# Optimization experiments

Measured on AMD Instinct MI355X. Metric: run time of the kernel, lower is better.

## Reference

```python
import jax, jax.numpy as jnp
import numpy as np

NUM_HEADS = 16
NUM_KV_HEADS = 8
HEAD_DIM = 256
HIDDEN = 2048
ROT_DIM = 64          # head_dim * partial_rotary_factor (0.25)
RMS_EPS = 1e-6
ROPE_THETA = 10000.0
SEQ = 2048


def _rmsnorm(x, weight=None):
    # Gemma RMSNorm: x * rsqrt(mean(x^2)+eps) * (1 + w); v_norm has no scale.
    var = jnp.mean(jnp.square(x), axis=-1, keepdims=True)
    n = x * jax.lax.rsqrt(var + RMS_EPS)
    if weight is not None:
        n = n * (1.0 + weight)
    return n


def _rope(x, positions):
    # Partial neox-style RoPE on the first ROT_DIM dims of each head.
    # x: [S, H, D]
    rot, rest = x[..., :ROT_DIM], x[..., ROT_DIM:]
    half = ROT_DIM // 2
    inv_freq = 1.0 / (ROPE_THETA ** (jnp.arange(0, ROT_DIM, 2, dtype=jnp.float32) / ROT_DIM))
    freqs = positions.astype(jnp.float32)[:, None] * inv_freq  # [S, half]
    cos = jnp.cos(freqs)[:, None, :]  # [S, 1, half]
    sin = jnp.sin(freqs)[:, None, :]
    x1, x2 = rot[..., :half], rot[..., half:]
    rot_out = jnp.concatenate([x1 * cos - x2 * sin, x2 * cos + x1 * sin], axis=-1)
    return jnp.concatenate([rot_out, rest], axis=-1)


def setup_inputs() -> dict:
    key = jax.random.key(0)
    k1, k2, k3, k4, k5 = jax.random.split(key, 5)
    q_size = NUM_HEADS * HEAD_DIM
    kv_size = NUM_KV_HEADS * HEAD_DIM
    return {
        "positions": jnp.arange(SEQ, dtype=jnp.int32),
        "hidden_states": jax.random.normal(k1, (SEQ, HIDDEN), dtype=jnp.float32),
        "w_qkv": jax.random.normal(k2, (q_size + 2 * kv_size, HIDDEN), dtype=jnp.float32) * (HIDDEN ** -0.5),
        "q_norm_w": jax.random.normal(k3, (HEAD_DIM,), dtype=jnp.float32) * 0.02,
        "k_norm_w": jax.random.normal(k4, (HEAD_DIM,), dtype=jnp.float32) * 0.02,
        "w_o": jax.random.normal(k5, (HIDDEN, q_size), dtype=jnp.float32) * (q_size ** -0.5),
    }


def reference(positions, hidden_states, w_qkv, q_norm_w, k_norm_w, w_o):
    S = hidden_states.shape[0]
    q_size = NUM_HEADS * HEAD_DIM
    kv_size = NUM_KV_HEADS * HEAD_DIM

    qkv = hidden_states @ w_qkv.T  # [S, q+2kv]
    q, k, v = jnp.split(qkv, [q_size, q_size + kv_size], axis=-1)
    q = q.reshape(S, NUM_HEADS, HEAD_DIM)
    k = k.reshape(S, NUM_KV_HEADS, HEAD_DIM)
    v = v.reshape(S, NUM_KV_HEADS, HEAD_DIM)

    # per-head RMSNorms (v_norm: scale_shift=0, with_scale=False -> pure norm)
    q = _rmsnorm(q, q_norm_w)
    k = _rmsnorm(k, k_norm_w)
    v = _rmsnorm(v, None)

    q = _rope(q, positions)
    k = _rope(k, positions)

    # GQA: repeat kv heads to match query heads
    rep = NUM_HEADS // NUM_KV_HEADS
    k = jnp.repeat(k, rep, axis=1)  # [S, H, D]
    v = jnp.repeat(v, rep, axis=1)

    # RadixAttention constructed with scaling=1.0 -> no 1/sqrt(d) scale
    scores = jnp.einsum("qhd,khd->hqk", q, k)  # [H, S, S]
    causal = positions[:, None] >= positions[None, :]  # [S, S]
    scores = jnp.where(causal[None, :, :], scores, jnp.float32(-1e30))
    attn = jax.nn.softmax(scores, axis=-1)
    out = jnp.einsum("hqk,khd->qhd", attn, v)  # [S, H, D]
    out = out.reshape(S, q_size)
    return out @ w_o.T  # [S, HIDDEN]
```

## Files before the change

kernel.cpp:

```cpp
#include <hip/hip_runtime.h>
#include <stdint.h>
#include <math.h>

#define SEQ 2048
#define HID 2048
#define NH 16
#define NKV 8
#define HD 256
#define QSZ 4096
#define QKVN 8192

typedef __attribute__((ext_vector_type(4))) float f32x4;
typedef _Float16 f16x8 __attribute__((ext_vector_type(8)));
typedef unsigned short u16;

__device__ __forceinline__ u16 f2h(float f) {
  _Float16 h = (_Float16)f;
  return __builtin_bit_cast(u16, h);
}
__device__ __forceinline__ float h2f(u16 b) {
  return (float)__builtin_bit_cast(_Float16, b);
}
__device__ __forceinline__ void glds16(const void* g, void* l) {
  __builtin_amdgcn_global_load_lds(
      (const __attribute__((address_space(1))) uint32_t*)g,
      (__attribute__((address_space(3))) uint32_t*)l, 16, 0, 0);
}

__global__ void cvt_f32_f16(const float* __restrict__ in, u16* __restrict__ out, int n4) {
  int i = blockIdx.x * 256 + threadIdx.x;
  if (i < n4) {
    float4 v = reinterpret_cast<const float4*>(in)[i];
    ushort4 o = make_ushort4(f2h(v.x), f2h(v.y), f2h(v.z), f2h(v.w));
    reinterpret_cast<ushort4*>(out)[i] = o;
  }
}

template <int F16OUT>
__global__ __launch_bounds__(256, 2) void gemm_bt(
    const u16* __restrict__ A, const u16* __restrict__ B, void* __restrict__ Cv,
    int M, int N, int K) {
  __shared__ __align__(16) u16 As[128 * 32];
  __shared__ __align__(16) u16 Bs[128 * 32];
  const int t = threadIdx.x;
  const int w = t >> 6, l = t & 63;
  const int bm = blockIdx.y * 128, bn = blockIdx.x * 128;
  const int wr = (w >> 1) * 64, wc = (w & 1) * 64;
  f32x4 acc[4][4] = {};

  const int arow = t >> 2;
  const int acol = (t & 3) * 8;
  const u16* Ag0 = A + (size_t)(bm + arow) * K + acol;
  const u16* Ag1 = A + (size_t)(bm + 64 + arow) * K + acol;
  const u16* Bg0 = B + (size_t)(bn + arow) * K + acol;
  const u16* Bg1 = B + (size_t)(bn + 64 + arow) * K + acol;
  u16* Al0 = As + w * 512;
  u16* Al1 = As + 2048 + w * 512;
  u16* Bl0 = Bs + w * 512;
  u16* Bl1 = Bs + 2048 + w * 512;

  const int lr = l & 15;
  const int lko = (l >> 4) * 8;

  for (int k0 = 0; k0 < K; k0 += 32) {
    __syncthreads();
    glds16(Ag0 + k0, Al0);
    glds16(Ag1 + k0, Al1);
    glds16(Bg0 + k0, Bl0);
    glds16(Bg1 + k0, Bl1);
    __syncthreads();
    f16x8 a[4], b[4];
#pragma unroll
    for (int m = 0; m < 4; ++m) a[m] = *(const f16x8*)&As[(wr + m * 16 + lr) * 32 + lko];
#pragma unroll
    for (int n = 0; n < 4; ++n) b[n] = *(const f16x8*)&Bs[(wc + n * 16 + lr) * 32 + lko];
#pragma unroll
    for (int m = 0; m < 4; ++m)
#pragma unroll
      for (int n = 0; n < 4; ++n)
        acc[m][n] = __builtin_amdgcn_mfma_f32_16x16x32_f16(a[m], b[n], acc[m][n], 0, 0, 0);
  }

#pragma unroll
  for (int m = 0; m < 4; ++m) {
#pragma unroll
    for (int n = 0; n < 4; ++n) {
      const int col = bn + wc + n * 16 + lr;
      const int row0 = bm + wr + m * 16 + (l >> 4) * 4;
#pragma unroll
      for (int j = 0; j < 4; ++j) {
        float vv = acc[m][n][j];
        if constexpr (F16OUT)
          ((u16*)Cv)[(size_t)(row0 + j) * N + col] = f2h(vv);
        else
          ((float*)Cv)[(size_t)(row0 + j) * N + col] = vv;
      }
    }
  }
}

__global__ void norm_rope(const u16* __restrict__ qkv, const float* __restrict__ qw,
                          const float* __restrict__ kw, const int* __restrict__ pos,
                          u16* __restrict__ qo, u16* __restrict__ ko, u16* __restrict__ vt) {
  const int b = blockIdx.x;
  const int s = b >> 5;
  const int slot = b & 31;
  const int l = threadIdx.x;
  const u16* row = qkv + (size_t)s * QKVN + slot * HD;
  ushort4 rv = *reinterpret_cast<const ushort4*>(row + l * 4);
  float x0 = h2f(rv.x), x1 = h2f(rv.y), x2 = h2f(rv.z), x3 = h2f(rv.w);
  float ss = x0 * x0 + x1 * x1 + x2 * x2 + x3 * x3;
#pragma unroll
  for (int mk = 32; mk; mk >>= 1) ss += __shfl_xor(ss, mk);
  const float rs = rsqrtf(ss * (1.0f / 256.0f) + 1e-6f);
  float n0, n1, n2, n3;
  if (slot < 16) {
    float4 wv = *reinterpret_cast<const float4*>(qw + l * 4);
    n0 = x0 * rs * (1.f + wv.x); n1 = x1 * rs * (1.f + wv.y);
    n2 = x2 * rs * (1.f + wv.z); n3 = x3 * rs * (1.f + wv.w);
  } else if (slot < 24) {
    float4 wv = *reinterpret_cast<const float4*>(kw + l * 4);
    n0 = x0 * rs * (1.f + wv.x); n1 = x1 * rs * (1.f + wv.y);
    n2 = x2 * rs * (1.f + wv.z); n3 = x3 * rs * (1.f + wv.w);
  } else {
    n0 = x0 * rs; n1 = x1 * rs; n2 = x2 * rs; n3 = x3 * rs;
  }
  if (slot < 24) {
    float p0 = __shfl_xor(n0, 8), p1 = __shfl_xor(n1, 8);
    float p2 = __shfl_xor(n2, 8), p3 = __shfl_xor(n3, 8);
    if (l < 16) {
      const double posd = (double)pos[s];
      float v[4] = {n0, n1, n2, n3};
      const float par[4] = {p0, p1, p2, p3};
#pragma unroll
      for (int i = 0; i < 4; ++i) {
        const int d = l * 4 + i;
        const int fi = d & 31;
        double inv = exp2(-(double)fi * (13.287712379549449 / 32.0));
        double ph = posd * inv;
        double tr = ph * 0.15915494309189535;
        tr -= floor(tr);
        float ang = (float)(tr * 6.283185307179586);
        float sn, cs;
        sincosf(ang, &sn, &cs);
        v[i] = (d < 32) ? (v[i] * cs - par[i] * sn) : (v[i] * cs + par[i] * sn);
      }
      n0 = v[0]; n1 = v[1]; n2 = v[2]; n3 = v[3];
    }
  }
  if (slot < 16) {
    ushort4 o = make_ushort4(f2h(n0), f2h(n1), f2h(n2), f2h(n3));
    *reinterpret_cast<ushort4*>(qo + ((size_t)slot * SEQ + s) * HD + l * 4) = o;
  } else if (slot < 24) {
    ushort4 o = make_ushort4(f2h(n0), f2h(n1), f2h(n2), f2h(n3));
    *reinterpret_cast<ushort4*>(ko + ((size_t)(slot - 16) * SEQ + s) * HD + l * 4) = o;
  } else {
    u16* base = vt + (size_t)(slot - 24) * HD * SEQ + s;
    base[(size_t)(l * 4 + 0) * SEQ] = f2h(n0);
    base[(size_t)(l * 4 + 1) * SEQ] = f2h(n1);
    base[(size_t)(l * 4 + 2) * SEQ] = f2h(n2);
    base[(size_t)(l * 4 + 3) * SEQ] = f2h(n3);
  }
}

__global__ __launch_bounds__(256, 1) void attn_fwd(
    const u16* __restrict__ Q, const u16* __restrict__ Kb,
    const u16* __restrict__ Vt, u16* __restrict__ O) {
  __shared__ __align__(16) u16 Ks[2][64 * 256];
  __shared__ __align__(16) u16 Vs[2][256 * 64];
  __shared__ __align__(16) u16 Ps[4 * 32 * 72];
  const int t = threadIdx.x, w = t >> 6, l = t & 63;
  const int bq = (gridDim.x - 1) - blockIdx.x;
  const int h = blockIdx.y;
  const int hk = h >> 1;
  const int lr = l & 15, lg = l >> 4;

  f16x8 qf[2][8];
#pragma unroll
  for (int mi = 0; mi < 2; ++mi) {
    const u16* qrow =
        Q + ((size_t)h * SEQ + bq * 128 + w * 32 + mi * 16 + lr) * HD + lg * 8;
#pragma unroll
    for (int c = 0; c < 8; ++c) qf[mi][c] = *(const f16x8*)(qrow + c * 32);
  }

  float m[2][4], lsum[2][4];
#pragma unroll
  for (int mi = 0; mi < 2; ++mi)
#pragma unroll
    for (int j = 0; j < 4; ++j) { m[mi][j] = -1e30f; lsum[mi][j] = 0.f; }
  f32x4 oacc[2][16] = {};

  const u16* Kg = Kb + (size_t)hk * SEQ * HD;
  const u16* Vg = Vt + (size_t)hk * HD * SEQ;

  auto STAGE = [&](int tt, int buf) {
    const int kv0 = tt * 64;
#pragma unroll
    for (int i = 0; i < 8; ++i) {
      const int seg = i * 4 + w;
      const int r = 2 * seg + (l >> 5);
      const int c = (l & 31) ^ (r & 7);
      glds16(Kg + (size_t)(kv0 + r) * HD + c * 8, &Ks[buf][seg * 512]);
    }
#pragma unroll
    for (int i = 0; i < 8; ++i) {
      const int seg = i * 4 + w;
      const int d = seg * 8 + (l >> 3);
      const int c = (l & 7) ^ (d & 7);
      glds16(Vg + (size_t)d * SEQ + kv0 + c * 8, &Vs[buf][seg * 512]);
    }
  };

  const int nt = (bq + 1) * 2;
  STAGE(0, 0);
  int cur = 0;

  for (int tt = 0; tt < nt; ++tt) {
    if (tt + 1 < nt) {
      STAGE(tt + 1, cur ^ 1);
      asm volatile("s_waitcnt vmcnt(16)" ::: "memory");
    } else {
      asm volatile("s_waitcnt vmcnt(0)" ::: "memory");
    }
    __builtin_amdgcn_s_barrier();

    const int kv0 = tt * 64;
    const u16* Kc = &Ks[cur][0];
    const u16* Vc = &Vs[cur][0];

    f32x4 sv[2][4];
    __builtin_amdgcn_s_setprio(1);
#pragma unroll
    for (int n = 0; n < 4; ++n) {
      f32x4 s0 = {}, s1 = {};
      const int krow = n * 16 + lr;
      const int rb = krow * 256;
      const int sw = krow & 7;
#pragma unroll
      for (int c = 0; c < 8; ++c) {
        const int chunk = (c * 4 + lg) ^ sw;
        f16x8 kf = *(const f16x8*)&Kc[rb + chunk * 8];
        s0 = __builtin_amdgcn_mfma_f32_16x16x32_f16(qf[0][c], kf, s0, 0, 0, 0);
        s1 = __builtin_amdgcn_mfma_f32_16x16x32_f16(qf[1][c], kf, s1, 0, 0, 0);
      }
      sv[0][n] = s0;
      sv[1][n] = s1;
    }
    __builtin_amdgcn_s_setprio(0);
#pragma unroll
    for (int mi = 0; mi < 2; ++mi) {
      const int row0 = bq * 128 + w * 32 + mi * 16;
      if (kv0 + 63 > row0) {
        const int qrow0 = row0 + lg * 4;
#pragma unroll
        for (int n = 0; n < 4; ++n) {
          const int col = kv0 + n * 16 + lr;
#pragma unroll
          for (int j = 0; j < 4; ++j)
            if (col > qrow0 + j) sv[mi][n][j] = -1e30f;
        }
      }
    }
    float pvv[2][4][4];
#pragma unroll
    for (int mi = 0; mi < 2; ++mi) {
#pragma unroll
      for (int j = 0; j < 4; ++j) {
        float mx = fmaxf(fmaxf(sv[mi][0][j], sv[mi][1][j]),
                         fmaxf(sv[mi][2][j], sv[mi][3][j]));
#pragma unroll
        for (int mk = 8; mk; mk >>= 1) mx = fmaxf(mx, __shfl_xor(mx, mk));
        if (mx > m[mi][j] + 8.f) {
          const float scale = __expf(m[mi][j] - mx);
          m[mi][j] = mx;
          lsum[mi][j] *= scale;
#pragma unroll
          for (int nc = 0; nc < 16; ++nc) oacc[mi][nc][j] *= scale;
        }
        float rsum = 0.f;
#pragma unroll
        for (int n = 0; n < 4; ++n) {
          float e = __expf(sv[mi][n][j] - m[mi][j]);
          pvv[mi][n][j] = e;
          rsum += e;
        }
#pragma unroll
        for (int mk = 8; mk; mk >>= 1) rsum += __shfl_xor(rsum, mk);
        lsum[mi][j] += rsum;
      }
    }
    u16* pb = Ps + w * 2304;
#pragma unroll
    for (int mi = 0; mi < 2; ++mi)
#pragma unroll
      for (int n = 0; n < 4; ++n)
#pragma unroll
        for (int j = 0; j < 4; ++j)
          pb[(mi * 16 + lg * 4 + j) * 72 + n * 16 + lr] = f2h(pvv[mi][n][j]);
    __builtin_amdgcn_s_setprio(1);
#pragma unroll
    for (int kk = 0; kk < 2; ++kk) {
      f16x8 pa0 = *(const f16x8*)&pb[(lr)*72 + kk * 32 + lg * 8];
      f16x8 pa1 = *(const f16x8*)&pb[(16 + lr) * 72 + kk * 32 + lg * 8];
#pragma unroll
      for (int nc = 0; nc < 16; ++nc) {
        const int drow = nc * 16 + lr;
        const int chunk = (kk * 4 + lg) ^ (drow & 7);
        f16x8 vf = *(const f16x8*)&Vc[drow * 64 + chunk * 8];
        oacc[0][nc] = __builtin_amdgcn_mfma_f32_16x16x32_f16(pa0, vf, oacc[0][nc], 0, 0, 0);
        oacc[1][nc] = __builtin_amdgcn_mfma_f32_16x16x32_f16(pa1, vf, oacc[1][nc], 0, 0, 0);
      }
    }
    __builtin_amdgcn_s_setprio(0);
    __builtin_amdgcn_s_barrier();
    cur ^= 1;
  }
#pragma unroll
  for (int mi = 0; mi < 2; ++mi) {
    float rl[4];
#pragma unroll
    for (int j = 0; j < 4; ++j) rl[j] = __fdividef(1.f, lsum[mi][j]);
#pragma unroll
    for (int nc = 0; nc < 16; ++nc) {
#pragma unroll
      for (int j = 0; j < 4; ++j) {
        const int qr = bq * 128 + w * 32 + mi * 16 + lg * 4 + j;
        O[(size_t)qr * QSZ + h * HD + nc * 16 + lr] = f2h(oacc[mi][nc][j] * rl[j]);
      }
    }
  }
}

extern "C" void kernel_launch(void* const* d_in, const int* in_sizes, int n_in,
                              void* d_out, int out_size, void* d_ws, size_t ws_size,
                              hipStream_t stream) {
  const int* pos = (const int*)d_in[0];
  const float* hidden = (const float*)d_in[1];
  const float* wqkv = (const float*)d_in[2];
  const float* qw = (const float*)d_in[3];
  const float* kw = (const float*)d_in[4];
  const float* wo_f = (const float*)d_in[5];
  float* out = (float*)d_out;

  char* wsp = (char*)d_ws;
  u16* hb = (u16*)(wsp);
  u16* wqb = (u16*)(wsp + (8ll << 20));
  u16* wob = (u16*)(wsp + (40ll << 20));
  u16* qkvb = (u16*)(wsp + (56ll << 20));
  u16* qb = (u16*)(wsp);
  u16* kb = (u16*)(wsp + (16ll << 20));
  u16* vt = (u16*)(wsp + (24ll << 20));
  u16* ao = (u16*)(wsp + (56ll << 20));

  cvt_f32_f16<<<(HID * HID / 4 + 255) / 256, 256, 0, stream>>>(hidden, hb, HID * HID / 4);
  cvt_f32_f16<<<(QKVN * HID / 4 + 255) / 256, 256, 0, stream>>>(wqkv, wqb, QKVN * HID / 4);
  cvt_f32_f16<<<(HID * QSZ / 4 + 255) / 256, 256, 0, stream>>>(wo_f, wob, HID * QSZ / 4);

  gemm_bt<1><<<dim3(QKVN / 128, SEQ / 128), 256, 0, stream>>>(hb, wqb, (void*)qkvb, SEQ, QKVN, HID);
  norm_rope<<<SEQ * 32, 64, 0, stream>>>(qkvb, qw, kw, pos, qb, kb, vt);
  attn_fwd<<<dim3(SEQ / 128, NH), 256, 0, stream>>>(qb, kb, vt, ao);
  gemm_bt<0><<<dim3(HID / 128, SEQ / 128), 256, 0, stream>>>(ao, wob, (void*)out, SEQ, HID, QSZ);
}
```

Before: 444.1 us.

## Restructure attention into 64-row query tiles with register-resident P and split head dim

The attention kernel now uses 64-query blocks (32 per head instead of 16), with the four waves split into two row halves and two head-dimension halves. It computes S transposed so P can be packed into MFMA operands directly in registers, dropping the LDS round trip for P. It also switches to a single-buffered K/V stage with a full wait, removes the one-block-per-CU launch bound, and alternates causal block ordering across heads to balance load. Grid parallelism and occupancy go up, but each wave now recomputes QK^T for its row half twice (once per dg), and load/compute overlap from double buffering is lost.

```diff
diff --git a/kernel.cpp b/kernel.cpp
--- a/kernel.cpp
+++ b/kernel.cpp
@@ -12,6 +12,7 @@
 
 typedef __attribute__((ext_vector_type(4))) float f32x4;
 typedef _Float16 f16x8 __attribute__((ext_vector_type(8)));
+typedef _Float16 f16x4 __attribute__((ext_vector_type(4)));
 typedef unsigned short u16;
 
 __device__ __forceinline__ u16 f2h(float f) {
@@ -163,15 +164,17 @@
   }
 }
 
-__global__ __launch_bounds__(256, 1) void attn_fwd(
+__global__ __launch_bounds__(256) void attn_fwd(
     const u16* __restrict__ Q, const u16* __restrict__ Kb,
     const u16* __restrict__ Vt, u16* __restrict__ O) {
-  __shared__ __align__(16) u16 Ks[2][64 * 256];
-  __shared__ __align__(16) u16 Vs[2][256 * 64];
-  __shared__ __align__(16) u16 Ps[4 * 32 * 72];
+  __shared__ __align__(16) u16 Ks[64 * 256];
+  __shared__ __align__(16) u16 Vs[256 * 64];
   const int t = threadIdx.x, w = t >> 6, l = t & 63;
-  const int bq = (gridDim.x - 1) - blockIdx.x;
-  const int h = blockIdx.y;
+  const int dg = w & 1;
+  const int rh = w >> 1;
+  const int x = blockIdx.x, h = blockIdx.y;
+  const int flip = (h >> 3) & 1;
+  const int bq = flip ? x : (31 - x);
   const int hk = h >> 1;
   const int lr = l & 15, lg = l >> 4;
 
@@ -179,154 +182,150 @@
 #pragma unroll
   for (int mi = 0; mi < 2; ++mi) {
     const u16* qrow =
-        Q + ((size_t)h * SEQ + bq * 128 + w * 32 + mi * 16 + lr) * HD + lg * 8;
+        Q + ((size_t)h * SEQ + bq * 64 + rh * 32 + mi * 16 + lr) * HD + lg * 8;
 #pragma unroll
     for (int c = 0; c < 8; ++c) qf[mi][c] = *(const f16x8*)(qrow + c * 32);
   }
 
-  float m[2][4], lsum[2][4];
-#pragma unroll
-  for (int mi = 0; mi < 2; ++mi)
-#pragma unroll
-    for (int j = 0; j < 4; ++j) { m[mi][j] = -1e30f; lsum[mi][j] = 0.f; }
-  f32x4 oacc[2][16] = {};
+  float m[2] = {-1e30f, -1e30f}, lsum[2] = {0.f, 0.f};
+  f32x4 oacc[2][8] = {};
 
   const u16* Kg = Kb + (size_t)hk * SEQ * HD;
   const u16* Vg = Vt + (size_t)hk * HD * SEQ;
 
-  auto STAGE = [&](int tt, int buf) {
+  for (int tt = 0; tt <= bq; ++tt) {
     const int kv0 = tt * 64;
 #pragma unroll
     for (int i = 0; i < 8; ++i) {
       const int seg = i * 4 + w;
       const int r = 2 * seg + (l >> 5);
       const int c = (l & 31) ^ (r & 7);
-      glds16(Kg + (size_t)(kv0 + r) * HD + c * 8, &Ks[buf][seg * 512]);
+      glds16(Kg + (size_t)(kv0 + r) * HD + c * 8, Ks + seg * 512);
     }
 #pragma unroll
     for (int i = 0; i < 8; ++i) {
       const int seg = i * 4 + w;
       const int d = seg * 8 + (l >> 3);
       const int c = (l & 7) ^ (d & 7);
-      glds16(Vg + (size_t)d * SEQ + kv0 + c * 8, &Vs[buf][seg * 512]);
-    }
-  };
-
-  const int nt = (bq + 1) * 2;
-  STAGE(0, 0);
-  int cur = 0;
-
-  for (int tt = 0; tt < nt; ++tt) {
-    if (tt + 1 < nt) {
-      STAGE(tt + 1, cur ^ 1);
-      asm volatile("s_waitcnt vmcnt(16)" ::: "memory");
-    } else {
-      asm volatile("s_waitcnt vmcnt(0)" ::: "memory");
-    }
+      glds16(Vg + (size_t)d * SEQ + kv0 + c * 8, Vs + seg * 512);
+    }
+    asm volatile("s_waitcnt vmcnt(0)" ::: "memory");
     __builtin_amdgcn_s_barrier();
-
-    const int kv0 = tt * 64;
-    const u16* Kc = &Ks[cur][0];
-    const u16* Vc = &Vs[cur][0];
 
     f32x4 sv[2][4];
     __builtin_amdgcn_s_setprio(1);
 #pragma unroll
     for (int n = 0; n < 4; ++n) {
       f32x4 s0 = {}, s1 = {};
-      const int krow = n * 16 + lr;
-      const int rb = krow * 256;
-      const int sw = krow & 7;
+      const int rb = (n * 16 + lr) * 256;
+      const int sw = lr & 7;
 #pragma unroll
       for (int c = 0; c < 8; ++c) {
-        const int chunk = (c * 4 + lg) ^ sw;
-        f16x8 kf = *(const f16x8*)&Kc[rb + chunk * 8];
-        s0 = __builtin_amdgcn_mfma_f32_16x16x32_f16(qf[0][c], kf, s0, 0, 0, 0);
-        s1 = __builtin_amdgcn_mfma_f32_16x16x32_f16(qf[1][c], kf, s1, 0, 0, 0);
+        f16x8 kf = *(const f16x8*)&Ks[rb + (((c * 4 + lg) ^ sw) * 8)];
+        s0 = __builtin_amdgcn_mfma_f32_16x16x32_f16(kf, qf[0][c], s0, 0, 0, 0);
+        s1 = __builtin_amdgcn_mfma_f32_16x16x32_f16(kf, qf[1][c], s1, 0, 0, 0);
       }
       sv[0][n] = s0;
       sv[1][n] = s1;
     }
     __builtin_amdgcn_s_setprio(0);
+
+    if (tt == bq) {
+#pragma unroll
+      for (int mi = 0; mi < 2; ++mi) {
+        const int q = bq * 64 + rh * 32 + mi * 16 + lr;
+#pragma unroll
+        for (int n = 0; n < 4; ++n) {
+#pragma unroll
+          for (int j = 0; j < 4; ++j)
+            if (kv0 + n * 16 + lg * 4 + j > q) sv[mi][n][j] = -1e30f;
+        }
+      }
+    }
+
+    f16x8 pa[2][2];
 #pragma unroll
     for (int mi = 0; mi < 2; ++mi) {
-      const int row0 = bq * 128 + w * 32 + mi * 16;
-      if (kv0 + 63 > row0) {
-        const int qrow0 = row0 + lg * 4;
-#pragma unroll
-        for (int n = 0; n < 4; ++n) {
-          const int col = kv0 + n * 16 + lr;
-#pragma unroll
-          for (int j = 0; j < 4; ++j)
-            if (col > qrow0 + j) sv[mi][n][j] = -1e30f;
-        }
-      }
-    }
-    float pvv[2][4][4];
-#pragma unroll
-    for (int mi = 0; mi < 2; ++mi) {
-#pragma unroll
-      for (int j = 0; j < 4; ++j) {
-        float mx = fmaxf(fmaxf(sv[mi][0][j], sv[mi][1][j]),
-                         fmaxf(sv[mi][2][j], sv[mi][3][j]));
-#pragma unroll
-        for (int mk = 8; mk; mk >>= 1) mx = fmaxf(mx, __shfl_xor(mx, mk));
-        if (mx > m[mi][j] + 8.f) {
-          const float scale = __expf(m[mi][j] - mx);
-          m[mi][j] = mx;
-          lsum[mi][j] *= scale;
-#pragma unroll
-          for (int nc = 0; nc < 16; ++nc) oacc[mi][nc][j] *= scale;
-        }
-        float rsum = 0.f;
-#pragma unroll
-        for (int n = 0; n < 4; ++n) {
-          float e = __expf(sv[mi][n][j] - m[mi][j]);
-          pvv[mi][n][j] = e;
+      float mx = fmaxf(fmaxf(sv[mi][0][0], sv[mi][0][1]),
+                       fmaxf(sv[mi][0][2], sv[mi][0][3]));
+#pragma unroll
+      for (int n = 1; n < 4; ++n) {
+        mx = fmaxf(mx, fmaxf(fmaxf(sv[mi][n][0], sv[mi][n][1]),
+                             fmaxf(sv[mi][n][2], sv[mi][n][3])));
+      }
+      mx = fmaxf(mx, __shfl_xor(mx, 16));
+      mx = fmaxf(mx, __shfl_xor(mx, 32));
+      if (__any(mx > m[mi] + 8.f)) {
+        const float mn = fmaxf(m[mi], mx);
+        const float sc = __expf(m[mi] - mn);
+        m[mi] = mn;
+        lsum[mi] *= sc;
+        float st[4];
+#pragma unroll
+        for (int j = 0; j < 4; ++j) st[j] = __shfl(sc, (l & 48) + lg * 4 + j);
+#pragma unroll
+        for (int nc = 0; nc < 8; ++nc)
+#pragma unroll
+          for (int j = 0; j < 4; ++j) oacc[mi][nc][j] *= st[j];
+      }
+      float p[4][4];
+      float rsum = 0.f;
+#pragma unroll
+      for (int n = 0; n < 4; ++n)
+#pragma unroll
+        for (int j = 0; j < 4; ++j) {
+          float e = __expf(sv[mi][n][j] - m[mi]);
+          p[n][j] = e;
           rsum += e;
         }
-#pragma unroll
-        for (int mk = 8; mk; mk >>= 1) rsum += __shfl_xor(rsum, mk);
-        lsum[mi][j] += rsum;
-      }
-    }
-    u16* pb = Ps + w * 2304;
-#pragma unroll
-    for (int mi = 0; mi < 2; ++mi)
-#pragma unroll
-      for (int n = 0; n < 4; ++n)
-#pragma unroll
-        for (int j = 0; j < 4; ++j)
-          pb[(mi * 16 + lg * 4 + j) * 72 + n * 16 + lr] = f2h(pvv[mi][n][j]);
+      rsum += __shfl_xor(rsum, 16);
+      rsum += __shfl_xor(rsum, 32);
+      lsum[mi] += rsum;
+#pragma unroll
+      for (int kk = 0; kk < 2; ++kk) {
+        f16x8 v;
+#pragma unroll
+        for (int j = 0; j < 4; ++j) {
+          v[j] = (_Float16)p[2 * kk][j];
+          v[j + 4] = (_Float16)p[2 * kk + 1][j];
+        }
+        pa[mi][kk] = v;
+      }
+    }
+
     __builtin_amdgcn_s_setprio(1);
 #pragma unroll
     for (int kk = 0; kk < 2; ++kk) {
-      f16x8 pa0 = *(const f16x8*)&pb[(lr)*72 + kk * 32 + lg * 8];
-      f16x8 pa1 = *(const f16x8*)&pb[(16 + lr) * 72 + kk * 32 + lg * 8];
-#pragma unroll
-      for (int nc = 0; nc < 16; ++nc) {
-        const int drow = nc * 16 + lr;
-        const int chunk = (kk * 4 + lg) ^ (drow & 7);
-        f16x8 vf = *(const f16x8*)&Vc[drow * 64 + chunk * 8];
-        oacc[0][nc] = __builtin_amdgcn_mfma_f32_16x16x32_f16(pa0, vf, oacc[0][nc], 0, 0, 0);
-        oacc[1][nc] = __builtin_amdgcn_mfma_f32_16x16x32_f16(pa1, vf, oacc[1][nc], 0, 0, 0);
+#pragma unroll
+      for (int nc = 0; nc < 8; ++nc) {
+        const int d = dg * 128 + nc * 16 + lr;
+        const int base = d * 64;
+        const int dsw = d & 7;
+        const int g0 = 4 * kk + (lg >> 1);
+        f16x4 va = *(const f16x4*)&Vs[base + ((g0 ^ dsw) * 8) + (l & 16 ? 4 : 0)];
+        f16x4 vb = *(const f16x4*)&Vs[base + (((g0 + 2) ^ dsw) * 8) + (l & 16 ? 4 : 0)];
+        f16x8 vf = __builtin_shufflevector(va, vb, 0, 1, 2, 3, 4, 5, 6, 7);
+        oacc[0][nc] = __builtin_amdgcn_mfma_f32_16x16x32_f16(pa[0][kk], vf, oacc[0][nc], 0, 0, 0);
+        oacc[1][nc] = __builtin_amdgcn_mfma_f32_16x16x32_f16(pa[1][kk], vf, oacc[1][nc], 0, 0, 0);
       }
     }
     __builtin_amdgcn_s_setprio(0);
     __builtin_amdgcn_s_barrier();
-    cur ^= 1;
-  }
+  }
+
 #pragma unroll
   for (int mi = 0; mi < 2; ++mi) {
     float rl[4];
 #pragma unroll
-    for (int j = 0; j < 4; ++j) rl[j] = __fdividef(1.f, lsum[mi][j]);
-#pragma unroll
-    for (int nc = 0; nc < 16; ++nc) {
+    for (int j = 0; j < 4; ++j)
+      rl[j] = __fdividef(1.f, __shfl(lsum[mi], (l & 48) + lg * 4 + j));
+#pragma unroll
+    for (int nc = 0; nc < 8; ++nc) {
 #pragma unroll
       for (int j = 0; j < 4; ++j) {
-        const int qr = bq * 128 + w * 32 + mi * 16 + lg * 4 + j;
-        O[(size_t)qr * QSZ + h * HD + nc * 16 + lr] = f2h(oacc[mi][nc][j] * rl[j]);
+        const int q = bq * 64 + rh * 32 + mi * 16 + lg * 4 + j;
+        O[(size_t)q * QSZ + h * HD + dg * 128 + nc * 16 + lr] =
+            f2h(oacc[mi][nc][j] * rl[j]);
       }
     }
   }
@@ -359,6 +358,6 @@
 
   gemm_bt<1><<<dim3(QKVN / 128, SEQ / 128), 256, 0, stream>>>(hb, wqb, (void*)qkvb, SEQ, QKVN, HID);
   norm_rope<<<SEQ * 32, 64, 0, stream>>>(qkvb, qw, kw, pos, qb, kb, vt);
-  attn_fwd<<<dim3(SEQ / 128, NH), 256, 0, stream>>>(qb, kb, vt, ao);
+  attn_fwd<<<dim3(32, NH), 256, 0, stream>>>(qb, kb, vt, ao);
   gemm_bt<0><<<dim3(HID / 128, SEQ / 128), 256, 0, stream>>>(ao, wob, (void*)out, SEQ, HID, QSZ);
 }
```

Result: faster. 417.6 us (-6.0%).
